# Performance work log

Hardware: AMD Instinct MI355X
Metric: run time of the kernel (lower is better)

Reference implementation:

```python
import jax, jax.numpy as jnp
import numpy as np
from jax import lax

HEADS = 4
DIM = 64
GATE_HID = 16


def setup_inputs() -> dict:
    key = jax.random.key(0)
    ks = jax.random.split(key, 12)
    b, c, h, w = 2, DIM, 48, 48
    s = 0.05
    x = jax.random.normal(ks[0], (b, c, h, w), jnp.float32)
    Wqkv = jax.random.normal(ks[1], (3 * c, c), jnp.float32) * s
    bqkv = jax.random.normal(ks[2], (3 * c,), jnp.float32) * s
    Wpos = jax.random.normal(ks[3], (3 * c, 1, 3, 3), jnp.float32) * s
    bpos = jax.random.normal(ks[4], (3 * c,), jnp.float32) * s
    Wg1 = jax.random.normal(ks[5], (GATE_HID, 1), jnp.float32) * 0.5
    bg1 = jax.random.normal(ks[6], (GATE_HID,), jnp.float32) * 0.1
    Wg2 = jax.random.normal(ks[7], (1, GATE_HID), jnp.float32) * 0.5
    bg2 = jax.random.normal(ks[8], (1,), jnp.float32) * 0.1
    Wproj = jax.random.normal(ks[9], (c, c), jnp.float32) * s
    bproj = jax.random.normal(ks[10], (c,), jnp.float32) * s
    return {"x": x, "Wqkv": Wqkv, "bqkv": bqkv, "Wpos": Wpos, "bpos": bpos,
            "Wg1": Wg1, "bg1": bg1, "Wg2": Wg2, "bg2": bg2,
            "Wproj": Wproj, "bproj": bproj}


def _forward(x, Wqkv, bqkv, Wpos, bpos, Wg1, bg1, Wg2, bg2, Wproj, bproj):
    b, c, h, w = x.shape
    n = h * w
    heads = HEADS
    hd = c // heads
    scale = hd ** -0.5
    # qkv 1x1 conv then 3x3 depthwise positional conv
    qkv = jnp.einsum('bchw,oc->bohw', x, Wqkv) + bqkv[None, :, None, None]
    qkv = lax.conv_general_dilated(
        qkv, Wpos, window_strides=(1, 1), padding='SAME',
        feature_group_count=3 * c,
        dimension_numbers=('NCHW', 'OIHW', 'NCHW')) + bpos[None, :, None, None]
    q, k, v = jnp.split(qkv, 3, axis=1)

    def to_heads(t):
        # [b,c,h,w] -> [b,heads,n,hd]
        return t.reshape(b, c, n).transpose(0, 2, 1).reshape(b, n, heads, hd).transpose(0, 2, 1, 3)

    q, k, v = to_heads(q), to_heads(k), to_heads(v)
    attn = jnp.einsum('bhid,bhjd->bhij', q, k) * scale  # [b,heads,n,n]
    prob = jax.nn.softmax(attn, axis=-1)
    entropy = -(prob * jnp.log(jnp.clip(prob, 1e-12))).sum(-1).mean(-1)  # [b,heads]
    # entropy gate: sigmoid(fc2(relu(fc1(e)))) * 0.9 + 0.1
    hgate = jax.nn.relu(entropy[..., None] @ Wg1.T + bg1)  # [b,heads,16]
    ratio = jax.nn.sigmoid(hgate @ Wg2.T + bg2)[..., 0] * 0.9 + 0.1  # [b,heads]
    # dynamic per-(batch,head) top-k along rows via rank threshold
    keep = jnp.clip(jnp.ceil(ratio * n).astype(jnp.int32), 1, n)  # [b,heads]
    sorted_desc = -jnp.sort(-attn, axis=-1)  # [b,heads,n,n]
    idx = jnp.broadcast_to((keep - 1)[:, :, None, None], (b, heads, n, 1))
    thresh = jnp.take_along_axis(sorted_desc, idx, axis=-1)  # [b,heads,n,1]
    sparse = jnp.where(attn >= thresh, attn, -jnp.inf)
    p = jax.nn.softmax(sparse, axis=-1)
    out = jnp.einsum('bhij,bhjd->bhid', p, v)  # [b,heads,n,hd]
    out = out.transpose(0, 2, 1, 3).reshape(b, n, c)
    out = out @ Wproj.T + bproj
    return out.transpose(0, 2, 1).reshape(b, c, h, w)


def reference(x, Wqkv, bqkv, Wpos, bpos, Wg1, bg1, Wg2, bg2, Wproj, bproj):
    return _forward(x, Wqkv, bqkv, Wpos, bpos, Wg1, bg1, Wg2, bg2, Wproj, bproj)
```

## Files before the change

### kernel.cpp

```cpp
#include <hip/hip_runtime.h>
#include <hip/hip_fp16.h>


#define NEG_INF (-__builtin_huge_valf())

typedef _Float16 half8_t __attribute__((ext_vector_type(8)));
typedef float floatx4 __attribute__((ext_vector_type(4)));

__device__ __forceinline__ unsigned h2key(unsigned short u) {
  return (u & 0x8000u) ? (unsigned)((~u) & 0xFFFFu) : (unsigned)(u | 0x8000u);
}
__device__ __forceinline__ float key16_to_float(unsigned k) {
  unsigned short u = (k & 0x8000u) ? (unsigned short)(k & 0x7FFFu)
                                   : (unsigned short)((~k) & 0xFFFFu);
  return __half2float(__ushort_as_half(u));
}

__global__ __launch_bounds__(256) void k_qkv(const float* __restrict__ x,
                                             const float* __restrict__ W,
                                             const float* __restrict__ bias,
                                             float* __restrict__ out) {
  int blk = blockIdx.x;
  int chunk = blk % 9;
  int o = (blk / 9) % 192;
  int b = blk / (9 * 192);
  int pos = chunk * 256 + threadIdx.x;
  const float* xb = x + b * 64 * 2304 + pos;
  const float* wr = W + o * 64;
  float acc = bias[o];
#pragma unroll
  for (int c = 0; c < 64; c++) acc = fmaf(wr[c], xb[c * 2304], acc);
  out[(b * 192 + o) * 2304 + pos] = acc;
}

__global__ __launch_bounds__(256) void k_dw(const float* __restrict__ qkv,
                                            const float* __restrict__ Wpos,
                                            const float* __restrict__ bpos,
                                            _Float16* __restrict__ q2,
                                            _Float16* __restrict__ k2,
                                            float* __restrict__ vh) {
  int blk = blockIdx.x;
  int chunk = blk % 9;
  int ch = (blk / 9) % 192;
  int b = blk / (9 * 192);
  int pos = chunk * 256 + threadIdx.x;
  int yy = pos / 48, xx = pos % 48;
  const float* in = qkv + (b * 192 + ch) * 2304;
  const float* w = Wpos + ch * 9;
  float acc = bpos[ch];
#pragma unroll
  for (int dy = -1; dy <= 1; dy++) {
    int y2 = yy + dy;
    if ((unsigned)y2 < 48u) {
#pragma unroll
      for (int dx = -1; dx <= 1; dx++) {
        int x2 = xx + dx;
        if ((unsigned)x2 < 48u)
          acc = fmaf(w[(dy + 1) * 3 + (dx + 1)], in[y2 * 48 + x2], acc);
      }
    }
  }
  int sel = ch >> 6;
  int c = ch & 63;
  int head = c >> 4, d = c & 15;
  size_t idx = (size_t)(b * 4 + head) * 2304 + pos;
  if (sel == 2) {
    vh[idx * 16 + d] = acc;
  } else {
    if (sel == 0) acc *= 0.25f;
    _Float16 h1 = (_Float16)acc;
    float r = acc - (float)h1;
    _Float16 h2 = (_Float16)r;
    _Float16* dst = (sel == 0) ? q2 : k2;
    dst[idx * 32 + d] = h1;
    dst[idx * 32 + 16 + d] = h2;
  }
}

template <bool STORE>
__global__ __launch_bounds__(256) void k_ent_t(const _Float16* __restrict__ q2,
                                               const _Float16* __restrict__ k2,
                                               float* __restrict__ ent,
                                               uint2* __restrict__ lgG) {
  int blk = blockIdx.x;
  int rowtile = blk % 144;
  int bh = blk / 144;
  int row0 = rowtile * 16;
  int tid = threadIdx.x, lane = tid & 63, wave = tid >> 6;
  int m16 = lane & 15, quad = lane >> 4;

  const half8_t* q2v =
      (const half8_t*)(q2 + ((size_t)bh * 2304 + row0 + m16) * 32);
  half8_t A1 = q2v[quad];
  half8_t zh = {};
  half8_t A2 = (lane < 32) ? A1 : zh;
  const half8_t* kbase = (const half8_t*)(k2 + (size_t)bh * 2304 * 32);

  uint2* dstRow =
      STORE ? (lgG + ((size_t)bh * 576 + rowtile * 4 + quad) * 2304) : nullptr;

  float mreg[4] = {NEG_INF, NEG_INF, NEG_INF, NEG_INF};
#pragma unroll 4
  for (int t = 0; t < 36; t++) {
    int col = wave * 576 + t * 16 + m16;
    const half8_t* kk = kbase + (size_t)col * 4;
    half8_t b1 = kk[quad & 1];
    half8_t b2 = kk[2 + (quad & 1)];
    floatx4 acc = {};
    acc = __builtin_amdgcn_mfma_f32_16x16x32_f16(A2, b2, acc, 0, 0, 0);
    acc = __builtin_amdgcn_mfma_f32_16x16x32_f16(A1, b1, acc, 0, 0, 0);
#pragma unroll
    for (int i = 0; i < 4; i++) mreg[i] = fmaxf(mreg[i], acc[i]);
    if (STORE) {
      __half2 h01 = __floats2half2_rn(acc[0], acc[1]);
      __half2 h23 = __floats2half2_rn(acc[2], acc[3]);
      uint2 packed;
      packed.x = *(unsigned*)&h01;
      packed.y = *(unsigned*)&h23;
      dstRow[col] = packed;
    }
  }
#pragma unroll
  for (int off = 1; off < 16; off <<= 1)
#pragma unroll
    for (int i = 0; i < 4; i++)
      mreg[i] = fmaxf(mreg[i], __shfl_xor(mreg[i], off));

  __shared__ float mWv[4][16], sWv[4][16], uWv[4][16];
  if (m16 == 0) {
#pragma unroll
    for (int i = 0; i < 4; i++) mWv[wave][quad * 4 + i] = mreg[i];
  }
  __syncthreads();
  float mrow[4];
#pragma unroll
  for (int i = 0; i < 4; i++) {
    int r = quad * 4 + i;
    mrow[i] = fmaxf(fmaxf(mWv[0][r], mWv[1][r]), fmaxf(mWv[2][r], mWv[3][r]));
  }

  float s[4] = {0.f, 0.f, 0.f, 0.f}, u[4] = {0.f, 0.f, 0.f, 0.f};
#pragma unroll 4
  for (int t = 0; t < 36; t++) {
    int col = wave * 576 + t * 16 + m16;
    const half8_t* kk = kbase + (size_t)col * 4;
    half8_t b1 = kk[quad & 1];
    half8_t b2 = kk[2 + (quad & 1)];
    floatx4 acc = {};
    acc = __builtin_amdgcn_mfma_f32_16x16x32_f16(A2, b2, acc, 0, 0, 0);
    acc = __builtin_amdgcn_mfma_f32_16x16x32_f16(A1, b1, acc, 0, 0, 0);
#pragma unroll
    for (int i = 0; i < 4; i++) {
      float z = acc[i] - mrow[i];
      float e = __expf(z);
      s[i] += e;
      u[i] = fmaf(z, e, u[i]);
    }
  }
#pragma unroll
  for (int off = 1; off < 16; off <<= 1) {
#pragma unroll
    for (int i = 0; i < 4; i++) {
      s[i] += __shfl_xor(s[i], off);
      u[i] += __shfl_xor(u[i], off);
    }
  }
  if (m16 == 0) {
#pragma unroll
    for (int i = 0; i < 4; i++) {
      sWv[wave][quad * 4 + i] = s[i];
      uWv[wave][quad * 4 + i] = u[i];
    }
  }
  __syncthreads();
  if (tid < 16) {
    float S = sWv[0][tid] + sWv[1][tid] + sWv[2][tid] + sWv[3][tid];
    float U = uWv[0][tid] + uWv[1][tid] + uWv[2][tid] + uWv[3][tid];
    float er = __logf(S) - U / S;
    er += __shfl_xor(er, 1);
    er += __shfl_xor(er, 2);
    er += __shfl_xor(er, 4);
    er += __shfl_xor(er, 8);
    if (tid == 0) atomicAdd(&ent[bh], er);
  }
}

template <bool CACHED>
__global__ __launch_bounds__(256, 7) void k_attn_t(
    const _Float16* __restrict__ q2, const _Float16* __restrict__ k2,
    const float* __restrict__ vh, const uint2* __restrict__ lgG,
    const float* __restrict__ ent, const float* __restrict__ Wg1,
    const float* __restrict__ bg1, const float* __restrict__ Wg2,
    const float* __restrict__ bg2, float* __restrict__ oh) {
  __shared__ __align__(16) unsigned long long ldsRaw[18432 / 8];
  __shared__ float mSh[4][4];
  __shared__ float thSh[4];
  __shared__ float sShW[4][4];

  uint2* lgt64 = (uint2*)ldsRaw;
  const unsigned short* lgtU = (const unsigned short*)ldsRaw;

  int blk = blockIdx.x;
  int rowblk = blk % 576;
  int bh = blk / 576;
  int row0 = rowblk * 4;
  int tid = threadIdx.x, lane = tid & 63, wave = tid >> 6;

  const float4* vb = (const float4*)(vh + (size_t)bh * 2304 * 16);

  float eAvg = ent[bh] * (1.f / 2304.f);
  float gacc = bg2[0];
#pragma unroll
  for (int i = 0; i < 16; i++) {
    float h = fmaxf(fmaf(eAvg, Wg1[i], bg1[i]), 0.f);
    gacc = fmaf(h, Wg2[i], gacc);
  }
  float ratio = 0.9f / (1.f + __expf(-gacc)) + 0.1f;
  int kp = (int)ceilf(ratio * 2304.f);
  unsigned keep = (unsigned)min(max(kp, 1), 2304);

  float mloc[4] = {NEG_INF, NEG_INF, NEG_INF, NEG_INF};
  if (CACHED) {
    const uint2* src = lgG + (size_t)blk * 2304;
#pragma unroll
    for (int jj = 0; jj < 9; jj++) {
      int j = tid + jj * 256;
      uint2 raw = src[j];
      lgt64[j] = raw;
      float2 a01 = __half22float2(*(__half2*)&raw.x);
      float2 a23 = __half22float2(*(__half2*)&raw.y);
      mloc[0] = fmaxf(mloc[0], a01.x);
      mloc[1] = fmaxf(mloc[1], a01.y);
      mloc[2] = fmaxf(mloc[2], a23.x);
      mloc[3] = fmaxf(mloc[3], a23.y);
    }
  } else {
    int m16 = lane & 15, quad = lane >> 4;
    const half8_t* q2v =
        (const half8_t*)(q2 + ((size_t)bh * 2304 + row0 + (m16 & 3)) * 32);
    half8_t A1 = q2v[quad];
    half8_t zh = {};
    half8_t A2 = (lane < 32) ? A1 : zh;
    const half8_t* kbase = (const half8_t*)(k2 + (size_t)bh * 2304 * 32);
#pragma unroll 4
    for (int t = 0; t < 36; t++) {
      int ct = wave * 36 + t;
      int col = ct * 16 + m16;
      const half8_t* kk = kbase + (size_t)col * 4;
      half8_t b1 = kk[quad & 1];
      half8_t b2 = kk[2 + (quad & 1)];
      floatx4 acc = {};
      acc = __builtin_amdgcn_mfma_f32_16x16x32_f16(A2, b2, acc, 0, 0, 0);
      acc = __builtin_amdgcn_mfma_f32_16x16x32_f16(A1, b1, acc, 0, 0, 0);
      if (lane < 16) {
        int j = ct * 16 + lane;
        __half2 h01 = __floats2half2_rn(acc[0], acc[1]);
        __half2 h23 = __floats2half2_rn(acc[2], acc[3]);
        uint2 packed;
        packed.x = *(unsigned*)&h01;
        packed.y = *(unsigned*)&h23;
        lgt64[j] = packed;
#pragma unroll
        for (int i = 0; i < 4; i++) mloc[i] = fmaxf(mloc[i], acc[i]);
      }
    }
  }
#pragma unroll
  for (int off = 1; off < 64; off <<= 1)
#pragma unroll
    for (int r = 0; r < 4; r++)
      mloc[r] = fmaxf(mloc[r], __shfl_xor(mloc[r], off));
  if (lane == 0) {
#pragma unroll
    for (int r = 0; r < 4; r++) mSh[wave][r] = mloc[r];
  }
  __syncthreads();
  float m[4];
#pragma unroll
  for (int r = 0; r < 4; r++)
    m[r] = fmaxf(fmaxf(mSh[0][r], mSh[1][r]), fmaxf(mSh[2][r], mSh[3][r]));

  {
    int r = wave;
    unsigned keys[36];
#pragma unroll
    for (int i = 0; i < 36; i++) {
      int j = lane + i * 64;
      keys[i] = h2key(lgtU[j * 4 + r]);
    }
    unsigned T = 0u;
    for (int bit = 15; bit >= 0; --bit) {
      unsigned cand = T | (1u << bit);
      unsigned cnt = 0u;
#pragma unroll
      for (int i = 0; i < 36; i++)
        cnt += (unsigned)__popcll(__ballot(keys[i] >= cand));
      if (cnt >= keep) {
        T = cand;
        if (cnt == keep) break;
      }
    }
    if (lane == 0) thSh[r] = key16_to_float(T);
  }
  __syncthreads();
  float th[4];
#pragma unroll
  for (int r = 0; r < 4; r++) th[r] = thSh[r];

  float sp[4] = {0.f, 0.f, 0.f, 0.f};
#pragma unroll
  for (int jj = 0; jj < 9; jj++) {
    int j = tid + jj * 256;
    uint2 raw = lgt64[j];
    __half2 h01 = *(__half2*)&raw.x;
    __half2 h23 = *(__half2*)&raw.y;
    float2 a01 = __half22float2(h01);
    float2 a23 = __half22float2(h23);
    float av[4] = {a01.x, a01.y, a23.x, a23.y};
    float p[4];
#pragma unroll
    for (int r = 0; r < 4; r++) {
      p[r] = (av[r] >= th[r]) ? __expf(av[r] - m[r]) : 0.f;
      sp[r] += p[r];
    }
    __half2 p01 = __floats2half2_rn(p[0], p[1]);
    __half2 p23 = __floats2half2_rn(p[2], p[3]);
    uint2 packed;
    packed.x = *(unsigned*)&p01;
    packed.y = *(unsigned*)&p23;
    lgt64[j] = packed;
  }
#pragma unroll
  for (int off = 1; off < 64; off <<= 1)
#pragma unroll
    for (int r = 0; r < 4; r++) sp[r] += __shfl_xor(sp[r], off);
  if (lane == 0) {
#pragma unroll
    for (int r = 0; r < 4; r++) sShW[wave][r] = sp[r];
  }
  __syncthreads();

  int dg = tid & 3, jg = tid >> 2;
  float acc[4][4];
#pragma unroll
  for (int r = 0; r < 4; r++)
#pragma unroll
    for (int i = 0; i < 4; i++) acc[r][i] = 0.f;
  for (int jj = 0; jj < 36; jj++) {
    int j = jg + jj * 64;
    float4 v4 = vb[j * 4 + dg];
    uint2 raw = lgt64[j];
    float2 p01 = __half22float2(*(__half2*)&raw.x);
    float2 p23 = __half22float2(*(__half2*)&raw.y);
    float p[4] = {p01.x, p01.y, p23.x, p23.y};
#pragma unroll
    for (int r = 0; r < 4; r++) {
      acc[r][0] = fmaf(p[r], v4.x, acc[r][0]);
      acc[r][1] = fmaf(p[r], v4.y, acc[r][1]);
      acc[r][2] = fmaf(p[r], v4.z, acc[r][2]);
      acc[r][3] = fmaf(p[r], v4.w, acc[r][3]);
    }
  }

  __syncthreads();
  float* part = (float*)ldsRaw;
#pragma unroll
  for (int r = 0; r < 4; r++)
#pragma unroll
    for (int i = 0; i < 4; i++)
      part[jg * 65 + r * 16 + dg * 4 + i] = acc[r][i];
  __syncthreads();
  if (tid < 64) {
    float t2 = 0.f;
    for (int g = 0; g < 64; g++) t2 += part[g * 65 + tid];
    int r = tid >> 4, d = tid & 15;
    float S = sShW[0][r] + sShW[1][r] + sShW[2][r] + sShW[3][r];
    oh[((size_t)(bh * 2304 + row0 + r)) * 16 + d] = t2 / S;
  }
}

__global__ __launch_bounds__(256) void k_proj(const float* __restrict__ oh,
                                              const float* __restrict__ Wp,
                                              const float* __restrict__ bp,
                                              float* __restrict__ out) {
  int blk = blockIdx.x;
  int chunk = blk % 9;
  int co = (blk / 9) % 64;
  int b = blk / (9 * 64);
  int pos = chunk * 256 + threadIdx.x;
  const float* wr = Wp + co * 64;
  float acc = bp[co];
#pragma unroll
  for (int head = 0; head < 4; head++) {
    const float4* op = (const float4*)(oh + ((size_t)((b * 4 + head) * 2304 + pos)) * 16);
#pragma unroll
    for (int p = 0; p < 4; p++) {
      float4 o4 = op[p];
      acc = fmaf(wr[head * 16 + p * 4 + 0], o4.x, acc);
      acc = fmaf(wr[head * 16 + p * 4 + 1], o4.y, acc);
      acc = fmaf(wr[head * 16 + p * 4 + 2], o4.z, acc);
      acc = fmaf(wr[head * 16 + p * 4 + 3], o4.w, acc);
    }
  }
  out[(b * 64 + co) * 2304 + pos] = acc;
}

extern "C" void kernel_launch(void* const* d_in, const int* in_sizes, int n_in,
                              void* d_out, int out_size, void* d_ws,
                              size_t ws_size, hipStream_t stream) {
  const float* x    = (const float*)d_in[0];
  const float* Wqkv = (const float*)d_in[1];
  const float* bqkv = (const float*)d_in[2];
  const float* Wpos = (const float*)d_in[3];
  const float* bpos = (const float*)d_in[4];
  const float* Wg1  = (const float*)d_in[5];
  const float* bg1  = (const float*)d_in[6];
  const float* Wg2  = (const float*)d_in[7];
  const float* bg2  = (const float*)d_in[8];
  const float* Wpr  = (const float*)d_in[9];
  const float* bpr  = (const float*)d_in[10];
  float* out = (float*)d_out;

  const size_t lgBytes = (size_t)8 * 576 * 2304 * 8;
  const size_t baseBytes =
      (size_t)(884736 + 2 * 294912 + 8) * 4 + (size_t)2 * 589824 * 2;
  bool cached = ws_size >= lgBytes + baseBytes;

  char* base = (char*)d_ws;
  uint2* lgG = nullptr;
  if (cached) {
    lgG = (uint2*)base;
    base += lgBytes;
  }
  float* qkv_raw = (float*)base;
  float* vh = qkv_raw + 884736;
  float* oh = vh + 294912;
  float* ent = oh + 294912;
  _Float16* q2 = (_Float16*)(ent + 8);
  _Float16* k2 = q2 + 589824;

  (void)hipMemsetAsync(ent, 0, 8 * sizeof(float), stream);
  hipLaunchKernelGGL(k_qkv, dim3(2 * 192 * 9), dim3(256), 0, stream,
                     x, Wqkv, bqkv, qkv_raw);
  hipLaunchKernelGGL(k_dw, dim3(2 * 192 * 9), dim3(256), 0, stream,
                     qkv_raw, Wpos, bpos, q2, k2, vh);
  if (cached) {
    hipLaunchKernelGGL((k_ent_t<true>), dim3(8 * 144), dim3(256), 0, stream,
                       q2, k2, ent, lgG);
    hipLaunchKernelGGL((k_attn_t<true>), dim3(8 * 576), dim3(256), 0, stream,
                       q2, k2, vh, lgG, ent, Wg1, bg1, Wg2, bg2, oh);
  } else {
    hipLaunchKernelGGL((k_ent_t<false>), dim3(8 * 144), dim3(256), 0, stream,
                       q2, k2, ent, lgG);
    hipLaunchKernelGGL((k_attn_t<false>), dim3(8 * 576), dim3(256), 0, stream,
                       q2, k2, vh, lgG, ent, Wg1, bg1, Wg2, bg2, oh);
  }
  hipLaunchKernelGGL(k_proj, dim3(2 * 64 * 9), dim3(256), 0, stream,
                     oh, Wpr, bpr, out);
}
```

Baseline: 241.7 us.

## Use MFMA for P·V with fp16 transposed V and row-major logit cache

```diff
diff --git a/kernel.cpp b/kernel.cpp
--- a/kernel.cpp
+++ b/kernel.cpp
@@ -14,6 +14,39 @@
   unsigned short u = (k & 0x8000u) ? (unsigned short)(k & 0x7FFFu)
                                    : (unsigned short)((~k) & 0xFFFFu);
   return __half2float(__ushort_as_half(u));
+}
+
+__device__ __forceinline__ float max8(uint4 v, float mx) {
+  float2 f0 = __half22float2(*(__half2*)&v.x);
+  float2 f1 = __half22float2(*(__half2*)&v.y);
+  float2 f2 = __half22float2(*(__half2*)&v.z);
+  float2 f3 = __half22float2(*(__half2*)&v.w);
+  mx = fmaxf(mx, fmaxf(fmaxf(f0.x, f0.y), fmaxf(f1.x, f1.y)));
+  mx = fmaxf(mx, fmaxf(fmaxf(f2.x, f2.y), fmaxf(f3.x, f3.y)));
+  return mx;
+}
+
+__device__ __forceinline__ uint4 maskExp8(uint4 v, float th, float m,
+                                          float& sp) {
+  float2 f0 = __half22float2(*(__half2*)&v.x);
+  float2 f1 = __half22float2(*(__half2*)&v.y);
+  float2 f2 = __half22float2(*(__half2*)&v.z);
+  float2 f3 = __half22float2(*(__half2*)&v.w);
+  float p0 = (f0.x >= th) ? __expf(f0.x - m) : 0.f;
+  float p1 = (f0.y >= th) ? __expf(f0.y - m) : 0.f;
+  float p2 = (f1.x >= th) ? __expf(f1.x - m) : 0.f;
+  float p3 = (f1.y >= th) ? __expf(f1.y - m) : 0.f;
+  float p4 = (f2.x >= th) ? __expf(f2.x - m) : 0.f;
+  float p5 = (f2.y >= th) ? __expf(f2.y - m) : 0.f;
+  float p6 = (f3.x >= th) ? __expf(f3.x - m) : 0.f;
+  float p7 = (f3.y >= th) ? __expf(f3.y - m) : 0.f;
+  sp += ((p0 + p1) + (p2 + p3)) + ((p4 + p5) + (p6 + p7));
+  uint4 o;
+  __half2 h0 = __floats2half2_rn(p0, p1); o.x = *(unsigned*)&h0;
+  __half2 h1 = __floats2half2_rn(p2, p3); o.y = *(unsigned*)&h1;
+  __half2 h2 = __floats2half2_rn(p4, p5); o.z = *(unsigned*)&h2;
+  __half2 h3 = __floats2half2_rn(p6, p7); o.w = *(unsigned*)&h3;
+  return o;
 }
 
 __global__ __launch_bounds__(256) void k_qkv(const float* __restrict__ x,
@@ -38,7 +71,7 @@
                                             const float* __restrict__ bpos,
                                             _Float16* __restrict__ q2,
                                             _Float16* __restrict__ k2,
-                                            float* __restrict__ vh) {
+                                            _Float16* __restrict__ vt) {
   int blk = blockIdx.x;
   int chunk = blk % 9;
   int ch = (blk / 9) % 192;
@@ -63,11 +96,12 @@
   int sel = ch >> 6;
   int c = ch & 63;
   int head = c >> 4, d = c & 15;
-  size_t idx = (size_t)(b * 4 + head) * 2304 + pos;
+  int bh = b * 4 + head;
   if (sel == 2) {
-    vh[idx * 16 + d] = acc;
+    vt[((size_t)bh * 16 + d) * 2304 + pos] = (_Float16)acc;
   } else {
     if (sel == 0) acc *= 0.25f;
+    size_t idx = (size_t)bh * 2304 + pos;
     _Float16 h1 = (_Float16)acc;
     float r = acc - (float)h1;
     _Float16 h2 = (_Float16)r;
@@ -81,7 +115,10 @@
 __global__ __launch_bounds__(256) void k_ent_t(const _Float16* __restrict__ q2,
                                                const _Float16* __restrict__ k2,
                                                float* __restrict__ ent,
-                                               uint2* __restrict__ lgG) {
+                                               _Float16* __restrict__ lgH) {
+  __shared__ __align__(16) _Float16 tBuf[4][16][72];
+  __shared__ float mWv[4][16], sWv[4][16], uWv[4][16];
+
   int blk = blockIdx.x;
   int rowtile = blk % 144;
   int bh = blk / 144;
@@ -96,28 +133,35 @@
   half8_t A2 = (lane < 32) ? A1 : zh;
   const half8_t* kbase = (const half8_t*)(k2 + (size_t)bh * 2304 * 32);
 
-  uint2* dstRow =
-      STORE ? (lgG + ((size_t)bh * 576 + rowtile * 4 + quad) * 2304) : nullptr;
-
   float mreg[4] = {NEG_INF, NEG_INF, NEG_INF, NEG_INF};
-#pragma unroll 4
-  for (int t = 0; t < 36; t++) {
-    int col = wave * 576 + t * 16 + m16;
-    const half8_t* kk = kbase + (size_t)col * 4;
-    half8_t b1 = kk[quad & 1];
-    half8_t b2 = kk[2 + (quad & 1)];
-    floatx4 acc = {};
-    acc = __builtin_amdgcn_mfma_f32_16x16x32_f16(A2, b2, acc, 0, 0, 0);
-    acc = __builtin_amdgcn_mfma_f32_16x16x32_f16(A1, b1, acc, 0, 0, 0);
-#pragma unroll
-    for (int i = 0; i < 4; i++) mreg[i] = fmaxf(mreg[i], acc[i]);
+  for (int g = 0; g < 9; g++) {
+#pragma unroll
+    for (int tt = 0; tt < 4; tt++) {
+      int t = g * 4 + tt;
+      int col = wave * 576 + t * 16 + m16;
+      const half8_t* kk = kbase + (size_t)col * 4;
+      half8_t b1 = kk[quad & 1];
+      half8_t b2 = kk[2 + (quad & 1)];
+      floatx4 acc = {};
+      acc = __builtin_amdgcn_mfma_f32_16x16x32_f16(A2, b2, acc, 0, 0, 0);
+      acc = __builtin_amdgcn_mfma_f32_16x16x32_f16(A1, b1, acc, 0, 0, 0);
+#pragma unroll
+      for (int i = 0; i < 4; i++) {
+        mreg[i] = fmaxf(mreg[i], acc[i]);
+        if (STORE) tBuf[wave][quad * 4 + i][tt * 16 + m16] = (_Float16)acc[i];
+      }
+    }
     if (STORE) {
-      __half2 h01 = __floats2half2_rn(acc[0], acc[1]);
-      __half2 h23 = __floats2half2_rn(acc[2], acc[3]);
-      uint2 packed;
-      packed.x = *(unsigned*)&h01;
-      packed.y = *(unsigned*)&h23;
-      dstRow[col] = packed;
+      __syncthreads();
+      int rb = lane >> 3, seg = lane & 7;
+#pragma unroll
+      for (int it = 0; it < 2; it++) {
+        int rr = it * 8 + rb;
+        uint4 vv = *(const uint4*)&tBuf[wave][rr][seg * 8];
+        *(uint4*)(lgH + ((size_t)bh * 2304 + row0 + rr) * 2304 + wave * 576 +
+                  g * 64 + seg * 8) = vv;
+      }
+      __syncthreads();
     }
   }
 #pragma unroll
@@ -125,8 +169,6 @@
 #pragma unroll
     for (int i = 0; i < 4; i++)
       mreg[i] = fmaxf(mreg[i], __shfl_xor(mreg[i], off));
-
-  __shared__ float mWv[4][16], sWv[4][16], uWv[4][16];
   if (m16 == 0) {
 #pragma unroll
     for (int i = 0; i < 4; i++) mWv[wave][quad * 4 + i] = mreg[i];
@@ -188,17 +230,14 @@
 template <bool CACHED>
 __global__ __launch_bounds__(256, 7) void k_attn_t(
     const _Float16* __restrict__ q2, const _Float16* __restrict__ k2,
-    const float* __restrict__ vh, const uint2* __restrict__ lgG,
+    const _Float16* __restrict__ vt, const _Float16* __restrict__ lgH,
     const float* __restrict__ ent, const float* __restrict__ Wg1,
     const float* __restrict__ bg1, const float* __restrict__ Wg2,
     const float* __restrict__ bg2, float* __restrict__ oh) {
-  __shared__ __align__(16) unsigned long long ldsRaw[18432 / 8];
-  __shared__ float mSh[4][4];
-  __shared__ float thSh[4];
-  __shared__ float sShW[4][4];
-
-  uint2* lgt64 = (uint2*)ldsRaw;
-  const unsigned short* lgtU = (const unsigned short*)ldsRaw;
+  __shared__ __align__(16) _Float16 pbuf[4][2320];
+  __shared__ float sS[4];
+  __shared__ float mShF[4][4];
+  __shared__ __align__(16) float redSh[4][64];
 
   int blk = blockIdx.x;
   int rowblk = blk % 576;
@@ -206,8 +245,6 @@
   int row0 = rowblk * 4;
   int tid = threadIdx.x, lane = tid & 63, wave = tid >> 6;
 
-  const float4* vb = (const float4*)(vh + (size_t)bh * 2304 * 16);
-
   float eAvg = ent[bh] * (1.f / 2304.f);
   float gacc = bg2[0];
 #pragma unroll
@@ -219,21 +256,27 @@
   int kp = (int)ceilf(ratio * 2304.f);
   unsigned keep = (unsigned)min(max(kp, 1), 2304);
 
-  float mloc[4] = {NEG_INF, NEG_INF, NEG_INF, NEG_INF};
+  float m;
+  uint4* dst4 = (uint4*)pbuf[wave];
   if (CACHED) {
-    const uint2* src = lgG + (size_t)blk * 2304;
-#pragma unroll
-    for (int jj = 0; jj < 9; jj++) {
-      int j = tid + jj * 256;
-      uint2 raw = src[j];
-      lgt64[j] = raw;
-      float2 a01 = __half22float2(*(__half2*)&raw.x);
-      float2 a23 = __half22float2(*(__half2*)&raw.y);
-      mloc[0] = fmaxf(mloc[0], a01.x);
-      mloc[1] = fmaxf(mloc[1], a01.y);
-      mloc[2] = fmaxf(mloc[2], a23.x);
-      mloc[3] = fmaxf(mloc[3], a23.y);
-    }
+    const uint4* src =
+        (const uint4*)(lgH + ((size_t)bh * 2304 + row0 + wave) * 2304);
+    float mx = NEG_INF;
+#pragma unroll
+    for (int it = 0; it < 4; it++) {
+      int idx = lane + it * 64;
+      uint4 v = src[idx];
+      dst4[idx] = v;
+      mx = max8(v, mx);
+    }
+    if (lane < 32) {
+      uint4 v = src[256 + lane];
+      dst4[256 + lane] = v;
+      mx = max8(v, mx);
+    }
+#pragma unroll
+    for (int off = 1; off < 64; off <<= 1) mx = fmaxf(mx, __shfl_xor(mx, off));
+    m = mx;
   } else {
     int m16 = lane & 15, quad = lane >> 4;
     const half8_t* q2v =
@@ -242,6 +285,7 @@
     half8_t zh = {};
     half8_t A2 = (lane < 32) ? A1 : zh;
     const half8_t* kbase = (const half8_t*)(k2 + (size_t)bh * 2304 * 32);
+    float ml[4] = {NEG_INF, NEG_INF, NEG_INF, NEG_INF};
 #pragma unroll 4
     for (int t = 0; t < 36; t++) {
       int ct = wave * 36 + t;
@@ -253,41 +297,32 @@
       acc = __builtin_amdgcn_mfma_f32_16x16x32_f16(A2, b2, acc, 0, 0, 0);
       acc = __builtin_amdgcn_mfma_f32_16x16x32_f16(A1, b1, acc, 0, 0, 0);
       if (lane < 16) {
-        int j = ct * 16 + lane;
-        __half2 h01 = __floats2half2_rn(acc[0], acc[1]);
-        __half2 h23 = __floats2half2_rn(acc[2], acc[3]);
-        uint2 packed;
-        packed.x = *(unsigned*)&h01;
-        packed.y = *(unsigned*)&h23;
-        lgt64[j] = packed;
-#pragma unroll
-        for (int i = 0; i < 4; i++) mloc[i] = fmaxf(mloc[i], acc[i]);
+#pragma unroll
+        for (int i = 0; i < 4; i++) {
+          pbuf[i][ct * 16 + lane] = (_Float16)acc[i];
+          ml[i] = fmaxf(ml[i], acc[i]);
+        }
       }
     }
-  }
-#pragma unroll
-  for (int off = 1; off < 64; off <<= 1)
-#pragma unroll
-    for (int r = 0; r < 4; r++)
-      mloc[r] = fmaxf(mloc[r], __shfl_xor(mloc[r], off));
-  if (lane == 0) {
-#pragma unroll
-    for (int r = 0; r < 4; r++) mSh[wave][r] = mloc[r];
-  }
-  __syncthreads();
-  float m[4];
-#pragma unroll
-  for (int r = 0; r < 4; r++)
-    m[r] = fmaxf(fmaxf(mSh[0][r], mSh[1][r]), fmaxf(mSh[2][r], mSh[3][r]));
-
+#pragma unroll
+    for (int off = 1; off < 16; off <<= 1)
+#pragma unroll
+      for (int i = 0; i < 4; i++) ml[i] = fmaxf(ml[i], __shfl_xor(ml[i], off));
+    if (lane == 0) {
+#pragma unroll
+      for (int i = 0; i < 4; i++) mShF[wave][i] = ml[i];
+    }
+    __syncthreads();
+    m = fmaxf(fmaxf(mShF[0][wave], mShF[1][wave]),
+              fmaxf(mShF[2][wave], mShF[3][wave]));
+  }
+
+  float th;
   {
-    int r = wave;
+    const unsigned short* prow = (const unsigned short*)pbuf[wave];
     unsigned keys[36];
 #pragma unroll
-    for (int i = 0; i < 36; i++) {
-      int j = lane + i * 64;
-      keys[i] = h2key(lgtU[j * 4 + r]);
-    }
+    for (int i = 0; i < 36; i++) keys[i] = h2key(prow[lane + i * 64]);
     unsigned T = 0u;
     for (int bit = 15; bit >= 0; --bit) {
       unsigned cand = T | (1u << bit);
@@ -300,82 +335,49 @@
         if (cnt == keep) break;
       }
     }
-    if (lane == 0) thSh[r] = key16_to_float(T);
+    th = key16_to_float(T);
+  }
+
+  {
+    float sp = 0.f;
+#pragma unroll
+    for (int it = 0; it < 4; it++) {
+      int idx = lane + it * 64;
+      dst4[idx] = maskExp8(dst4[idx], th, m, sp);
+    }
+    if (lane < 32) {
+      int idx = 256 + lane;
+      dst4[idx] = maskExp8(dst4[idx], th, m, sp);
+    }
+#pragma unroll
+    for (int off = 1; off < 64; off <<= 1) sp += __shfl_xor(sp, off);
+    if (lane == 0) sS[wave] = sp;
   }
   __syncthreads();
-  float th[4];
-#pragma unroll
-  for (int r = 0; r < 4; r++) th[r] = thSh[r];
-
-  float sp[4] = {0.f, 0.f, 0.f, 0.f};
-#pragma unroll
-  for (int jj = 0; jj < 9; jj++) {
-    int j = tid + jj * 256;
-    uint2 raw = lgt64[j];
-    __half2 h01 = *(__half2*)&raw.x;
-    __half2 h23 = *(__half2*)&raw.y;
-    float2 a01 = __half22float2(h01);
-    float2 a23 = __half22float2(h23);
-    float av[4] = {a01.x, a01.y, a23.x, a23.y};
-    float p[4];
-#pragma unroll
-    for (int r = 0; r < 4; r++) {
-      p[r] = (av[r] >= th[r]) ? __expf(av[r] - m[r]) : 0.f;
-      sp[r] += p[r];
-    }
-    __half2 p01 = __floats2half2_rn(p[0], p[1]);
-    __half2 p23 = __floats2half2_rn(p[2], p[3]);
-    uint2 packed;
-    packed.x = *(unsigned*)&p01;
-    packed.y = *(unsigned*)&p23;
-    lgt64[j] = packed;
-  }
-#pragma unroll
-  for (int off = 1; off < 64; off <<= 1)
-#pragma unroll
-    for (int r = 0; r < 4; r++) sp[r] += __shfl_xor(sp[r], off);
-  if (lane == 0) {
-#pragma unroll
-    for (int r = 0; r < 4; r++) sShW[wave][r] = sp[r];
-  }
-  __syncthreads();
-
-  int dg = tid & 3, jg = tid >> 2;
-  float acc[4][4];
-#pragma unroll
-  for (int r = 0; r < 4; r++)
-#pragma unroll
-    for (int i = 0; i < 4; i++) acc[r][i] = 0.f;
-  for (int jj = 0; jj < 36; jj++) {
-    int j = jg + jj * 64;
-    float4 v4 = vb[j * 4 + dg];
-    uint2 raw = lgt64[j];
-    float2 p01 = __half22float2(*(__half2*)&raw.x);
-    float2 p23 = __half22float2(*(__half2*)&raw.y);
-    float p[4] = {p01.x, p01.y, p23.x, p23.y};
-#pragma unroll
-    for (int r = 0; r < 4; r++) {
-      acc[r][0] = fmaf(p[r], v4.x, acc[r][0]);
-      acc[r][1] = fmaf(p[r], v4.y, acc[r][1]);
-      acc[r][2] = fmaf(p[r], v4.z, acc[r][2]);
-      acc[r][3] = fmaf(p[r], v4.w, acc[r][3]);
-    }
-  }
-
-  __syncthreads();
-  float* part = (float*)ldsRaw;
-#pragma unroll
-  for (int r = 0; r < 4; r++)
-#pragma unroll
-    for (int i = 0; i < 4; i++)
-      part[jg * 65 + r * 16 + dg * 4 + i] = acc[r][i];
+
+  {
+    int m16 = lane & 15, quad = lane >> 4;
+    const _Float16* vrow = vt + ((size_t)bh * 16 + m16) * 2304;
+    const _Float16* prow = pbuf[m16 & 3];
+    int jb0 = wave * 576 + quad * 8;
+    floatx4 acc = {};
+#pragma unroll 6
+    for (int t = 0; t < 18; t++) {
+      int jb = jb0 + t * 32;
+      half8_t a = *(const half8_t*)&prow[jb];
+      half8_t b = *(const half8_t*)&vrow[jb];
+      acc = __builtin_amdgcn_mfma_f32_16x16x32_f16(a, b, acc, 0, 0, 0);
+    }
+    if (lane < 16) {
+      *(floatx4*)&redSh[wave][m16 * 4] = acc;
+    }
+  }
   __syncthreads();
   if (tid < 64) {
-    float t2 = 0.f;
-    for (int g = 0; g < 64; g++) t2 += part[g * 65 + tid];
-    int r = tid >> 4, d = tid & 15;
-    float S = sShW[0][r] + sShW[1][r] + sShW[2][r] + sShW[3][r];
-    oh[((size_t)(bh * 2304 + row0 + r)) * 16 + d] = t2 / S;
+    int r = tid & 3, d = tid >> 2;
+    float s2 = redSh[0][d * 4 + r] + redSh[1][d * 4 + r] +
+               redSh[2][d * 4 + r] + redSh[3][d * 4 + r];
+    oh[((size_t)(bh * 2304 + row0 + r)) * 16 + d] = s2 / sS[r];
   }
 }
 
@@ -392,7 +394,8 @@
   float acc = bp[co];
 #pragma unroll
   for (int head = 0; head < 4; head++) {
-    const float4* op = (const float4*)(oh + ((size_t)((b * 4 + head) * 2304 + pos)) * 16);
+    const float4* op =
+        (const float4*)(oh + ((size_t)((b * 4 + head) * 2304 + pos)) * 16);
 #pragma unroll
     for (int p = 0; p < 4; p++) {
       float4 o4 = op[p];
@@ -421,39 +424,39 @@
   const float* bpr  = (const float*)d_in[10];
   float* out = (float*)d_out;
 
-  const size_t lgBytes = (size_t)8 * 576 * 2304 * 8;
-  const size_t baseBytes =
-      (size_t)(884736 + 2 * 294912 + 8) * 4 + (size_t)2 * 589824 * 2;
+  const size_t lgBytes = (size_t)8 * 2304 * 2304 * 2;
+  const size_t baseBytes = (size_t)(884736 + 294912 + 8) * 4 +
+                           (size_t)(2 * 589824 + 294912) * 2;
   bool cached = ws_size >= lgBytes + baseBytes;
 
   char* base = (char*)d_ws;
-  uint2* lgG = nullptr;
+  _Float16* lgH = nullptr;
   if (cached) {
-    lgG = (uint2*)base;
+    lgH = (_Float16*)base;
     base += lgBytes;
   }
   float* qkv_raw = (float*)base;
-  float* vh = qkv_raw + 884736;
-  float* oh = vh + 294912;
+  float* oh = qkv_raw + 884736;
   float* ent = oh + 294912;
   _Float16* q2 = (_Float16*)(ent + 8);
   _Float16* k2 = q2 + 589824;
+  _Float16* vt = k2 + 589824;
 
   (void)hipMemsetAsync(ent, 0, 8 * sizeof(float), stream);
   hipLaunchKernelGGL(k_qkv, dim3(2 * 192 * 9), dim3(256), 0, stream,
                      x, Wqkv, bqkv, qkv_raw);
   hipLaunchKernelGGL(k_dw, dim3(2 * 192 * 9), dim3(256), 0, stream,
-                     qkv_raw, Wpos, bpos, q2, k2, vh);
+                     qkv_raw, Wpos, bpos, q2, k2, vt);
   if (cached) {
     hipLaunchKernelGGL((k_ent_t<true>), dim3(8 * 144), dim3(256), 0, stream,
-                       q2, k2, ent, lgG);
+                       q2, k2, ent, lgH);
     hipLaunchKernelGGL((k_attn_t<true>), dim3(8 * 576), dim3(256), 0, stream,
-                       q2, k2, vh, lgG, ent, Wg1, bg1, Wg2, bg2, oh);
+                       q2, k2, vt, lgH, ent, Wg1, bg1, Wg2, bg2, oh);
   } else {
     hipLaunchKernelGGL((k_ent_t<false>), dim3(8 * 144), dim3(256), 0, stream,
-                       q2, k2, ent, lgG);
+                       q2, k2, ent, lgH);
     hipLaunchKernelGGL((k_attn_t<false>), dim3(8 * 576), dim3(256), 0, stream,
-                       q2, k2, vh, lgG, ent, Wg1, bg1, Wg2, bg2, oh);
+                       q2, k2, vt, lgH, ent, Wg1, bg1, Wg2, bg2, oh);
   }
   hipLaunchKernelGGL(k_proj, dim3(2 * 64 * 9), dim3(256), 0, stream,
                      oh, Wpr, bpr, out);
```

Measured after the change: 229.2 us. 1.05x faster.
